# Optimization experiments

Hardware: AMD Instinct MI355X
Metric: run time of the kernel (lower is better)

## Reference

```python
import jax, jax.numpy as jnp
import numpy as np

N_NODES = 100000
N_EDGES = 1600000
IN_CH = 128
HID = 128
OUT_CH = 16
N_GRAPHS = 64


def setup_inputs() -> dict:
    key = jax.random.key(0)
    ks = jax.random.split(key, 8)
    x = jax.random.normal(ks[0], (N_NODES, IN_CH), dtype=jnp.float32)
    edge_index = jax.random.randint(ks[1], (2, N_EDGES), 0, N_NODES, dtype=jnp.int64)
    batch = jnp.sort(jax.random.randint(ks[2], (N_NODES,), 0, N_GRAPHS, dtype=jnp.int64))
    s1 = 1.0 / np.sqrt(IN_CH)
    s2 = 1.0 / np.sqrt(HID)
    W1 = jax.random.uniform(ks[3], (IN_CH, HID), jnp.float32, -s1, s1)
    b1 = jnp.zeros((HID,), jnp.float32)
    W2 = jax.random.uniform(ks[4], (HID, HID), jnp.float32, -s2, s2)
    b2 = jnp.zeros((HID,), jnp.float32)
    Wfc = jax.random.uniform(ks[5], (HID, OUT_CH), jnp.float32, -s2, s2)
    bfc = jax.random.uniform(ks[6], (OUT_CH,), jnp.float32, -s2, s2)
    return {"x": x, "W1": W1, "b1": b1, "W2": W2, "b2": b2,
            "Wfc": Wfc, "bfc": bfc, "edge_index": edge_index, "batch": batch}


def _gcn_conv(x, W, b, src, dst, deg_inv_sqrt, deg_inv):
    # GCNConv with self-loops: out = D^-1/2 (A+I) D^-1/2 (x W) + b
    h = x @ W                                   # [N, H]
    norm = deg_inv_sqrt[src] * deg_inv_sqrt[dst]  # [E]
    agg = jax.ops.segment_sum(h[src] * norm[:, None], dst, num_segments=N_NODES)
    # self-loop term: deg_inv_sqrt[i]^2 * h[i]
    return agg + h * deg_inv[:, None] + b


def reference(x, W1, b1, W2, b2, Wfc, bfc, edge_index, batch):
    src, dst = edge_index[0], edge_index[1]
    # degree including self-loop
    deg = jax.ops.segment_sum(jnp.ones((N_EDGES,), jnp.float32), dst, num_segments=N_NODES) + 1.0
    deg_inv_sqrt = jax.lax.rsqrt(deg)
    deg_inv = 1.0 / deg
    h = jax.nn.relu(_gcn_conv(x, W1, b1, src, dst, deg_inv_sqrt, deg_inv))
    h = jax.nn.relu(_gcn_conv(h, W2, b2, src, dst, deg_inv_sqrt, deg_inv))
    # global mean pool over graphs
    sums = jax.ops.segment_sum(h, batch, num_segments=N_GRAPHS)          # [G, H]
    counts = jax.ops.segment_sum(jnp.ones((N_NODES,), jnp.float32), batch, num_segments=N_GRAPHS)
    pooled = sums / jnp.maximum(counts, 1.0)[:, None]
    return pooled @ Wfc + bfc
```

## Files before the change

### kernel.cpp

```cpp
#include <hip/hip_runtime.h>
#include <math.h>

#define NN 100000
#define NE 1600000
#define CH 128
#define OUTC 16
#define NG 64

#define CBSH 9
#define NCB 196
#define CHK 8192
#define MAXB 12288
#define PS 8

typedef __attribute__((ext_vector_type(8))) short bf16x8;
typedef __attribute__((ext_vector_type(4))) float f32x4;

__device__ __forceinline__ unsigned short f2bf(float f) {
    union { float f; unsigned u; } v; v.f = f;
    unsigned r = v.u + 0x7FFF + ((v.u >> 16) & 1);
    return (unsigned short)(r >> 16);
}
__device__ __forceinline__ float bflo(unsigned u) {
    union { unsigned u; float f; } v; v.u = u << 16; return v.f;
}
__device__ __forceinline__ float bfhi(unsigned u) {
    union { unsigned u; float f; } v; v.u = u & 0xffff0000u; return v.f;
}

__global__ void k_prep(const float* __restrict__ W1, const float* __restrict__ W2,
                       unsigned short* __restrict__ wt1, unsigned short* __restrict__ wt2,
                       const int* __restrict__ batch, int* __restrict__ gptr,
                       int* __restrict__ bcnt) {
    int i = blockIdx.x * 256 + threadIdx.x;
    if (i < CH * CH) {
        int k = i >> 7, n = i & 127;
        wt1[n * CH + k] = f2bf(W1[i]);
    } else if (i < 2 * CH * CH) {
        int j = i - CH * CH;
        int k = j >> 7, n = j & 127;
        wt2[n * CH + k] = f2bf(W2[j]);
    }
    if (i < NCB) bcnt[i] = 0;
    if (i < NN) {
        int b = batch[i];
        int prev = (i == 0) ? -1 : batch[i - 1];
        for (int g = prev + 1; g <= b; g++) gptr[g] = i;
        if (i == NN - 1) {
            for (int g = b + 1; g <= NG; g++) gptr[g] = NN;
        }
    }
}

__global__ __launch_bounds__(1024) void k_hist(const int* __restrict__ dst, int* __restrict__ bcnt) {
    __shared__ int h[NCB];
    int t = threadIdx.x;
    if (t < NCB) h[t] = 0;
    __syncthreads();
    int base = blockIdx.x * CHK;
#pragma unroll
    for (int i = 0; i < 8; i++) {
        int e = base + i * 1024 + t;
        if (e < NE) atomicAdd(&h[dst[e] >> CBSH], 1);
    }
    __syncthreads();
    if (t < NCB && h[t]) atomicAdd(&bcnt[t], h[t]);
}

__global__ __launch_bounds__(1024) void k_bscan(const int* __restrict__ bcnt, int* __restrict__ ebase,
                        int* __restrict__ gfill, float* __restrict__ pooled) {
    __shared__ int s[256];
    int t = threadIdx.x;
    if (t < 256) s[t] = (t < NCB) ? bcnt[t] : 0;
    __syncthreads();
    for (int off = 1; off < 256; off <<= 1) {
        int v = 0;
        if (t < 256 && t >= off) v = s[t - off];
        __syncthreads();
        if (t < 256) s[t] += v;
        __syncthreads();
    }
    if (t == 0) ebase[0] = 0;
    if (t < NCB) { ebase[t + 1] = s[t]; gfill[t] = 0; }
    for (int i = t; i < NG * CH; i += 1024) pooled[i] = 0.f;
}

__global__ __launch_bounds__(1024) void k_passA(const int* __restrict__ src, const int* __restrict__ dst,
                        const int* __restrict__ ebase, int* __restrict__ gfill,
                        unsigned* __restrict__ ebuf) {
    __shared__ unsigned lbuf[CHK];
    __shared__ unsigned char lbyte[CHK];
    __shared__ int hcnt[NCB];
    __shared__ int hbase[256];
    __shared__ int goff[NCB];
    int t = threadIdx.x;
    if (t < NCB) hcnt[t] = 0;
    __syncthreads();
    int base = blockIdx.x * CHK;
    int cb[8], slot[8]; unsigned pk[8];
#pragma unroll
    for (int i = 0; i < 8; i++) {
        int e = base + i * 1024 + t;
        cb[i] = -1;
        if (e < NE) {
            int d = dst[e], s = src[e];
            cb[i] = d >> CBSH;
            pk[i] = ((unsigned)s << CBSH) | (unsigned)(d & 511);
            slot[i] = atomicAdd(&hcnt[cb[i]], 1);
        }
    }
    __syncthreads();
    if (t < 256) hbase[t] = (t < NCB) ? hcnt[t] : 0;
    __syncthreads();
    for (int off = 1; off < 256; off <<= 1) {
        int v = 0;
        if (t < 256 && t >= off) v = hbase[t - off];
        __syncthreads();
        if (t < 256) hbase[t] += v;
        __syncthreads();
    }
    if (t < NCB) {
        int c = hcnt[t];
        int g = c ? atomicAdd(&gfill[t], c) : 0;
        goff[t] = ebase[t] + g - (hbase[t] - c);
    }
    __syncthreads();
#pragma unroll
    for (int i = 0; i < 8; i++) {
        if (cb[i] >= 0) {
            int pos = hbase[cb[i]] - hcnt[cb[i]] + slot[i];
            lbuf[pos] = pk[i];
            lbyte[pos] = (unsigned char)cb[i];
        }
    }
    __syncthreads();
    int total = min(NE - base, CHK);
    for (int p = t; p < total; p += 1024) {
        unsigned v = lbuf[p];
        int b = lbyte[p];
        ebuf[goff[b] + p] = v;
    }
}

__global__ __launch_bounds__(1024) void k_passB(const unsigned* __restrict__ ebuf, const int* __restrict__ ebase,
                        int* __restrict__ degi, int* __restrict__ rowst,
                        float* __restrict__ dis, int* __restrict__ csr) {
    __shared__ int cnt[512];
    __shared__ int nbase[512];
    __shared__ int fill[512];
    __shared__ int stage[MAXB];
    int t = threadIdx.x;
    int cb = blockIdx.x;
    int nb0 = cb << CBSH;
    int ncnt = min(512, NN - nb0);
    int e0 = ebase[cb], e1 = ebase[cb + 1];
    if (t < 512) { cnt[t] = 0; fill[t] = 0; }
    __syncthreads();
    for (int e = e0 + t; e < e1; e += 1024)
        atomicAdd(&cnt[ebuf[e] & 511], 1);
    __syncthreads();
    if (t < 512) nbase[t] = cnt[t];
    __syncthreads();
    for (int off = 1; off < 512; off <<= 1) {
        int v = 0;
        if (t < 512 && t >= off) v = nbase[t - off];
        __syncthreads();
        if (t < 512) nbase[t] += v;
        __syncthreads();
    }
    for (int e = e0 + t; e < e1; e += 1024) {
        unsigned v = ebuf[e];
        int local = v & 511;
        int s = atomicAdd(&fill[local], 1);
        stage[nbase[local] - cnt[local] + s] = (int)(v >> CBSH);
    }
    __syncthreads();
    int total = e1 - e0;
    for (int p = t; p < total; p += 1024) csr[e0 + p] = stage[p];
    if (t < ncnt) {
        int c = cnt[t];
        degi[nb0 + t] = c;
        rowst[nb0 + t] = e0 + nbase[t] - c;
        dis[nb0 + t] = rsqrtf((float)c + 1.0f);
    }
}

template<bool F32IN>
__launch_bounds__(256, 2)
__global__ void k_gemm(const void* __restrict__ Av,
                       const unsigned short* __restrict__ WT,
                       const float* __restrict__ dis,
                       unsigned short* __restrict__ out) {
    int tid = threadIdx.x;
    int wave = tid >> 6, lane = tid & 63;
    int quad = lane >> 4, l16 = lane & 15;

    int rbase = blockIdx.x * 128 + wave * 32;

    bf16x8 af[2][4];
#pragma unroll
    for (int s = 0; s < 2; s++) {
        int row = rbase + s * 16 + l16;
        if (row >= NN) row = NN - 1;
        if (F32IN) {
            const float* arow = (const float*)Av + (size_t)row * CH + quad * 8;
#pragma unroll
            for (int ks = 0; ks < 4; ks++) {
                float4 lo = *(const float4*)(arow + ks * 32);
                float4 hi = *(const float4*)(arow + ks * 32 + 4);
                union { bf16x8 v; unsigned short u[8]; } tmp;
                tmp.u[0] = f2bf(lo.x); tmp.u[1] = f2bf(lo.y);
                tmp.u[2] = f2bf(lo.z); tmp.u[3] = f2bf(lo.w);
                tmp.u[4] = f2bf(hi.x); tmp.u[5] = f2bf(hi.y);
                tmp.u[6] = f2bf(hi.z); tmp.u[7] = f2bf(hi.w);
                af[s][ks] = tmp.v;
            }
        } else {
            const unsigned short* arow = (const unsigned short*)Av + (size_t)row * CH + quad * 8;
#pragma unroll
            for (int ks = 0; ks < 4; ks++) af[s][ks] = *(const bf16x8*)(arow + ks * 32);
        }
    }

    f32x4 acc[2][8];
#pragma unroll
    for (int s = 0; s < 2; s++)
#pragma unroll
        for (int t = 0; t < 8; t++) acc[s][t] = (f32x4){0.f, 0.f, 0.f, 0.f};

#pragma unroll
    for (int t = 0; t < 8; t++) {
        const unsigned short* wcol = WT + (size_t)(t * 16 + l16) * CH + quad * 8;
        bf16x8 b0 = *(const bf16x8*)(wcol);
        bf16x8 b1 = *(const bf16x8*)(wcol + 32);
        bf16x8 b2 = *(const bf16x8*)(wcol + 64);
        bf16x8 b3 = *(const bf16x8*)(wcol + 96);
#pragma unroll
        for (int s = 0; s < 2; s++) {
            acc[s][t] = __builtin_amdgcn_mfma_f32_16x16x32_bf16(af[s][0], b0, acc[s][t], 0, 0, 0);
            acc[s][t] = __builtin_amdgcn_mfma_f32_16x16x32_bf16(af[s][1], b1, acc[s][t], 0, 0, 0);
            acc[s][t] = __builtin_amdgcn_mfma_f32_16x16x32_bf16(af[s][2], b2, acc[s][t], 0, 0, 0);
            acc[s][t] = __builtin_amdgcn_mfma_f32_16x16x32_bf16(af[s][3], b3, acc[s][t], 0, 0, 0);
        }
    }

#pragma unroll
    for (int s = 0; s < 2; s++) {
#pragma unroll
        for (int r = 0; r < 4; r++) {
            int orow = rbase + s * 16 + quad * 4 + r;
            if (orow < NN) {
                float d = dis[orow];
#pragma unroll
                for (int t = 0; t < 8; t++) {
                    out[(size_t)orow * CH + t * 16 + l16] = f2bf(acc[s][t][r] * d);
                }
            }
        }
    }
}

__global__ __launch_bounds__(256) void k_agg(const unsigned short* __restrict__ ht, const int* __restrict__ rowst,
                      const int* __restrict__ degi, const int* __restrict__ csr,
                      const float* __restrict__ dis, const float* __restrict__ bias,
                      unsigned short* __restrict__ out) {
    int t = threadIdx.x;
    int grp = t >> 4;
    int q = t & 15;
    int n = blockIdx.x * 16 + grp;
    const uint4* base = (const uint4*)ht;

    uint4 sv = base[(size_t)n * 16 + q];
    float a[8];
    a[0] = bflo(sv.x); a[1] = bfhi(sv.x);
    a[2] = bflo(sv.y); a[3] = bfhi(sv.y);
    a[4] = bflo(sv.z); a[5] = bfhi(sv.z);
    a[6] = bflo(sv.w); a[7] = bfhi(sv.w);

    int start = rowst[n];
    int c = degi[n];
    int nb = c & ~7;
    int j = 0;
    for (; j < nb; j += 8) {
        int idx[8];
#pragma unroll
        for (int u = 0; u < 8; u++) idx[u] = csr[start + j + u];
        uint4 v[8];
#pragma unroll
        for (int u = 0; u < 8; u++) v[u] = base[(size_t)idx[u] * 16 + q];
#pragma unroll
        for (int u = 0; u < 8; u++) {
            a[0] += bflo(v[u].x); a[1] += bfhi(v[u].x);
            a[2] += bflo(v[u].y); a[3] += bfhi(v[u].y);
            a[4] += bflo(v[u].z); a[5] += bfhi(v[u].z);
            a[6] += bflo(v[u].w); a[7] += bfhi(v[u].w);
        }
    }
    if (j < c) {
        int idx[8];
#pragma unroll
        for (int u = 0; u < 8; u++) { int e = j + u; idx[u] = csr[start + (e < c ? e : c - 1)]; }
        uint4 v[8];
#pragma unroll
        for (int u = 0; u < 8; u++) v[u] = base[(size_t)idx[u] * 16 + q];
#pragma unroll
        for (int u = 0; u < 8; u++) {
            if (j + u < c) {
                a[0] += bflo(v[u].x); a[1] += bfhi(v[u].x);
                a[2] += bflo(v[u].y); a[3] += bfhi(v[u].y);
                a[4] += bflo(v[u].z); a[5] += bfhi(v[u].z);
                a[6] += bflo(v[u].w); a[7] += bfhi(v[u].w);
            }
        }
    }

    float d = dis[n];
    const float4* bp = (const float4*)bias;
    float4 b0 = bp[q * 2], b1 = bp[q * 2 + 1];
    uint4 o;
    {
        float ox = fmaxf(fmaf(d, a[0], b0.x), 0.f), oy = fmaxf(fmaf(d, a[1], b0.y), 0.f);
        o.x = ((unsigned)f2bf(oy) << 16) | (unsigned)f2bf(ox);
        ox = fmaxf(fmaf(d, a[2], b0.z), 0.f); oy = fmaxf(fmaf(d, a[3], b0.w), 0.f);
        o.y = ((unsigned)f2bf(oy) << 16) | (unsigned)f2bf(ox);
        ox = fmaxf(fmaf(d, a[4], b1.x), 0.f); oy = fmaxf(fmaf(d, a[5], b1.y), 0.f);
        o.z = ((unsigned)f2bf(oy) << 16) | (unsigned)f2bf(ox);
        ox = fmaxf(fmaf(d, a[6], b1.z), 0.f); oy = fmaxf(fmaf(d, a[7], b1.w), 0.f);
        o.w = ((unsigned)f2bf(oy) << 16) | (unsigned)f2bf(ox);
    }
    ((uint4*)out)[(size_t)n * 16 + q] = o;
}

__global__ __launch_bounds__(512) void k_pool2(const unsigned short* __restrict__ h,
                                               const int* __restrict__ gptr,
                                               float* __restrict__ pooled) {
    int g = blockIdx.x >> 3;
    int s = blockIdx.x & 7;
    int gs = gptr[g], ge = gptr[g + 1];
    int len = ge - gs;
    int i0 = gs + (int)(((long long)len * s) >> 3);
    int i1 = gs + (int)(((long long)len * (s + 1)) >> 3);
    int t = threadIdx.x;
    int pr = t & 63;
    int ro = t >> 6;
    const unsigned* base = (const unsigned*)h;
    float s0 = 0.f, s1 = 0.f;
    for (int n = i0 + ro; n < i1; n += 8) {
        unsigned v = base[(size_t)n * 64 + pr];
        s0 += bflo(v); s1 += bfhi(v);
    }
    __shared__ float red[2][8][64];
    red[0][ro][pr] = s0; red[1][ro][pr] = s1;
    __syncthreads();
    for (int off = 4; off >= 1; off >>= 1) {
        if (ro < off) {
            red[0][ro][pr] += red[0][ro + off][pr];
            red[1][ro][pr] += red[1][ro + off][pr];
        }
        __syncthreads();
    }
    if (ro == 0) {
        atomicAdd(&pooled[g * CH + pr * 2],     red[0][0][pr]);
        atomicAdd(&pooled[g * CH + pr * 2 + 1], red[1][0][pr]);
    }
}

__global__ void k_final(const float* __restrict__ pooled, const int* __restrict__ gptr,
                        const float* __restrict__ Wfc, const float* __restrict__ bfc,
                        float* __restrict__ out) {
    int idx = blockIdx.x * 256 + threadIdx.x;
    if (idx >= NG * OUTC) return;
    int g = idx >> 4, o = idx & 15;
    float c = (float)(gptr[g + 1] - gptr[g]);
    float inv = 1.0f / fmaxf(c, 1.0f);
    float s = 0.f;
    for (int k = 0; k < CH; k++) s += pooled[g * CH + k] * Wfc[k * OUTC + o];
    out[idx] = fmaf(s, inv, bfc[o]);
}

extern "C" void kernel_launch(void* const* d_in, const int* in_sizes, int n_in,
                              void* d_out, int out_size, void* d_ws, size_t ws_size,
                              hipStream_t stream) {
    (void)in_sizes; (void)n_in; (void)out_size; (void)ws_size;
    const float* x   = (const float*)d_in[0];
    const float* W1  = (const float*)d_in[1];
    const float* b1  = (const float*)d_in[2];
    const float* W2  = (const float*)d_in[3];
    const float* b2  = (const float*)d_in[4];
    const float* Wfc = (const float*)d_in[5];
    const float* bfc = (const float*)d_in[6];
    const int* ei    = (const int*)d_in[7];
    const int* batch = (const int*)d_in[8];
    const int* esrc = ei;
    const int* edst = ei + NE;
    float* out = (float*)d_out;

    char* w = (char*)d_ws;
    unsigned short* bufA = (unsigned short*)w; w += (size_t)NN * CH * 2;
    unsigned short* bufB = (unsigned short*)w; w += (size_t)NN * CH * 2;
    unsigned short* wt1  = (unsigned short*)w; w += (size_t)CH * CH * 2;
    unsigned short* wt2  = (unsigned short*)w; w += (size_t)CH * CH * 2;
    unsigned* ebuf = (unsigned*)w; w += (size_t)NE * 4;
    int* csr    = (int*)w;    w += (size_t)NE * 4;
    int* degi   = (int*)w;    w += (size_t)NN * 4;
    int* rowst  = (int*)w;    w += (size_t)NN * 4;
    float* dis  = (float*)w;  w += (size_t)NN * 4;
    int* bcnt   = (int*)w;    w += NCB * 4;
    int* ebase  = (int*)w;    w += (NCB + 1) * 4;
    int* gfill  = (int*)w;    w += NCB * 4;
    int* gptr   = (int*)w;    w += (NG + 1) * 4;
    float* pooled = (float*)w; w += (size_t)NG * CH * 4;

    const int histBlocks = (NE + CHK - 1) / CHK;
    const int gemmBlocks = (NN + 127) / 128;
    const int aggBlocks  = NN / 16;

    k_prep<<<(NN + 255) / 256, 256, 0, stream>>>(W1, W2, wt1, wt2, batch, gptr, bcnt);
    k_hist<<<histBlocks, 1024, 0, stream>>>(edst, bcnt);
    k_bscan<<<1, 1024, 0, stream>>>(bcnt, ebase, gfill, pooled);
    k_passA<<<histBlocks, 1024, 0, stream>>>(esrc, edst, ebase, gfill, ebuf);
    k_passB<<<NCB, 1024, 0, stream>>>(ebuf, ebase, degi, rowst, dis, csr);

    k_gemm<true><<<gemmBlocks, 256, 0, stream>>>(x, wt1, dis, bufA);
    k_agg<<<aggBlocks, 256, 0, stream>>>(bufA, rowst, degi, csr, dis, b1, bufB);
    k_gemm<false><<<gemmBlocks, 256, 0, stream>>>(bufB, wt2, dis, bufA);
    k_agg<<<aggBlocks, 256, 0, stream>>>(bufA, rowst, degi, csr, dis, b2, bufB);

    k_pool2<<<NG * PS, 512, 0, stream>>>(bufB, gptr, pooled);
    k_final<<<(NG * OUTC + 255) / 256, 256, 0, stream>>>(pooled, gptr, Wfc, bfc, out);
}
```

Baseline: 319.2 us.

## Fuse layer-1 GEMM, edge histogram and prep into one heterogeneous launch

Merges the first-layer GEMM (with W1 transposed and converted into shared memory per block), the destination-bucket histogram (now written as per-block partials), and the prep work into a single kernel whose blocks pick a role by block index. The layer-1 GEMM no longer depends on the CSR build or on dis, so it runs alongside the edge preprocessing. A new aggregation variant k_agg_w applies the source-side dis weights per edge, since the GEMM output is now unscaled. The cost is that every GEMM block redoes the W1 transpose into LDS, and the single-block bscan now has to sum 196 partial histograms.

```diff
diff --git a/kernel.cpp b/kernel.cpp
--- a/kernel.cpp
+++ b/kernel.cpp
@@ -12,6 +12,11 @@
 #define CHK 8192
 #define MAXB 12288
 #define PS 8
+#define LDA 136
+
+#define GEMMB 782
+#define HISTB 196
+#define PREPB 391
 
 typedef __attribute__((ext_vector_type(8))) short bf16x8;
 typedef __attribute__((ext_vector_type(4))) float f32x4;
@@ -28,182 +33,37 @@
     union { unsigned u; float f; } v; v.u = u & 0xffff0000u; return v.f;
 }
 
-__global__ void k_prep(const float* __restrict__ W1, const float* __restrict__ W2,
-                       unsigned short* __restrict__ wt1, unsigned short* __restrict__ wt2,
-                       const int* __restrict__ batch, int* __restrict__ gptr,
-                       int* __restrict__ bcnt) {
-    int i = blockIdx.x * 256 + threadIdx.x;
-    if (i < CH * CH) {
-        int k = i >> 7, n = i & 127;
-        wt1[n * CH + k] = f2bf(W1[i]);
-    } else if (i < 2 * CH * CH) {
-        int j = i - CH * CH;
-        int k = j >> 7, n = j & 127;
-        wt2[n * CH + k] = f2bf(W2[j]);
-    }
-    if (i < NCB) bcnt[i] = 0;
-    if (i < NN) {
-        int b = batch[i];
-        int prev = (i == 0) ? -1 : batch[i - 1];
-        for (int g = prev + 1; g <= b; g++) gptr[g] = i;
-        if (i == NN - 1) {
-            for (int g = b + 1; g <= NG; g++) gptr[g] = NN;
-        }
-    }
-}
-
-__global__ __launch_bounds__(1024) void k_hist(const int* __restrict__ dst, int* __restrict__ bcnt) {
-    __shared__ int h[NCB];
-    int t = threadIdx.x;
-    if (t < NCB) h[t] = 0;
-    __syncthreads();
-    int base = blockIdx.x * CHK;
-#pragma unroll
-    for (int i = 0; i < 8; i++) {
-        int e = base + i * 1024 + t;
-        if (e < NE) atomicAdd(&h[dst[e] >> CBSH], 1);
-    }
-    __syncthreads();
-    if (t < NCB && h[t]) atomicAdd(&bcnt[t], h[t]);
-}
-
-__global__ __launch_bounds__(1024) void k_bscan(const int* __restrict__ bcnt, int* __restrict__ ebase,
-                        int* __restrict__ gfill, float* __restrict__ pooled) {
-    __shared__ int s[256];
-    int t = threadIdx.x;
-    if (t < 256) s[t] = (t < NCB) ? bcnt[t] : 0;
-    __syncthreads();
-    for (int off = 1; off < 256; off <<= 1) {
-        int v = 0;
-        if (t < 256 && t >= off) v = s[t - off];
-        __syncthreads();
-        if (t < 256) s[t] += v;
-        __syncthreads();
-    }
-    if (t == 0) ebase[0] = 0;
-    if (t < NCB) { ebase[t + 1] = s[t]; gfill[t] = 0; }
-    for (int i = t; i < NG * CH; i += 1024) pooled[i] = 0.f;
-}
-
-__global__ __launch_bounds__(1024) void k_passA(const int* __restrict__ src, const int* __restrict__ dst,
-                        const int* __restrict__ ebase, int* __restrict__ gfill,
-                        unsigned* __restrict__ ebuf) {
-    __shared__ unsigned lbuf[CHK];
-    __shared__ unsigned char lbyte[CHK];
-    __shared__ int hcnt[NCB];
-    __shared__ int hbase[256];
-    __shared__ int goff[NCB];
-    int t = threadIdx.x;
-    if (t < NCB) hcnt[t] = 0;
-    __syncthreads();
-    int base = blockIdx.x * CHK;
-    int cb[8], slot[8]; unsigned pk[8];
-#pragma unroll
-    for (int i = 0; i < 8; i++) {
-        int e = base + i * 1024 + t;
-        cb[i] = -1;
-        if (e < NE) {
-            int d = dst[e], s = src[e];
-            cb[i] = d >> CBSH;
-            pk[i] = ((unsigned)s << CBSH) | (unsigned)(d & 511);
-            slot[i] = atomicAdd(&hcnt[cb[i]], 1);
-        }
-    }
-    __syncthreads();
-    if (t < 256) hbase[t] = (t < NCB) ? hcnt[t] : 0;
-    __syncthreads();
-    for (int off = 1; off < 256; off <<= 1) {
-        int v = 0;
-        if (t < 256 && t >= off) v = hbase[t - off];
-        __syncthreads();
-        if (t < 256) hbase[t] += v;
-        __syncthreads();
-    }
-    if (t < NCB) {
-        int c = hcnt[t];
-        int g = c ? atomicAdd(&gfill[t], c) : 0;
-        goff[t] = ebase[t] + g - (hbase[t] - c);
-    }
-    __syncthreads();
-#pragma unroll
-    for (int i = 0; i < 8; i++) {
-        if (cb[i] >= 0) {
-            int pos = hbase[cb[i]] - hcnt[cb[i]] + slot[i];
-            lbuf[pos] = pk[i];
-            lbyte[pos] = (unsigned char)cb[i];
-        }
-    }
-    __syncthreads();
-    int total = min(NE - base, CHK);
-    for (int p = t; p < total; p += 1024) {
-        unsigned v = lbuf[p];
-        int b = lbyte[p];
-        ebuf[goff[b] + p] = v;
-    }
-}
-
-__global__ __launch_bounds__(1024) void k_passB(const unsigned* __restrict__ ebuf, const int* __restrict__ ebase,
-                        int* __restrict__ degi, int* __restrict__ rowst,
-                        float* __restrict__ dis, int* __restrict__ csr) {
-    __shared__ int cnt[512];
-    __shared__ int nbase[512];
-    __shared__ int fill[512];
-    __shared__ int stage[MAXB];
-    int t = threadIdx.x;
-    int cb = blockIdx.x;
-    int nb0 = cb << CBSH;
-    int ncnt = min(512, NN - nb0);
-    int e0 = ebase[cb], e1 = ebase[cb + 1];
-    if (t < 512) { cnt[t] = 0; fill[t] = 0; }
-    __syncthreads();
-    for (int e = e0 + t; e < e1; e += 1024)
-        atomicAdd(&cnt[ebuf[e] & 511], 1);
-    __syncthreads();
-    if (t < 512) nbase[t] = cnt[t];
-    __syncthreads();
-    for (int off = 1; off < 512; off <<= 1) {
-        int v = 0;
-        if (t < 512 && t >= off) v = nbase[t - off];
-        __syncthreads();
-        if (t < 512) nbase[t] += v;
-        __syncthreads();
-    }
-    for (int e = e0 + t; e < e1; e += 1024) {
-        unsigned v = ebuf[e];
-        int local = v & 511;
-        int s = atomicAdd(&fill[local], 1);
-        stage[nbase[local] - cnt[local] + s] = (int)(v >> CBSH);
-    }
-    __syncthreads();
-    int total = e1 - e0;
-    for (int p = t; p < total; p += 1024) csr[e0 + p] = stage[p];
-    if (t < ncnt) {
-        int c = cnt[t];
-        degi[nb0 + t] = c;
-        rowst[nb0 + t] = e0 + nbase[t] - c;
-        dis[nb0 + t] = rsqrtf((float)c + 1.0f);
-    }
-}
-
-template<bool F32IN>
 __launch_bounds__(256, 2)
-__global__ void k_gemm(const void* __restrict__ Av,
-                       const unsigned short* __restrict__ WT,
-                       const float* __restrict__ dis,
-                       unsigned short* __restrict__ out) {
-    int tid = threadIdx.x;
-    int wave = tid >> 6, lane = tid & 63;
-    int quad = lane >> 4, l16 = lane & 15;
-
-    int rbase = blockIdx.x * 128 + wave * 32;
-
-    bf16x8 af[2][4];
-#pragma unroll
-    for (int s = 0; s < 2; s++) {
-        int row = rbase + s * 16 + l16;
-        if (row >= NN) row = NN - 1;
-        if (F32IN) {
-            const float* arow = (const float*)Av + (size_t)row * CH + quad * 8;
+__global__ void k_fused0(const float* __restrict__ x, const float* __restrict__ W1,
+                         const float* __restrict__ W2,
+                         unsigned short* __restrict__ wt2,
+                         const int* __restrict__ batch, int* __restrict__ gptr,
+                         int* __restrict__ gfill, float* __restrict__ pooled,
+                         const int* __restrict__ edst, int* __restrict__ hpart,
+                         unsigned short* __restrict__ bufA) {
+    __shared__ unsigned short wlds[128 * LDA];
+    int b = blockIdx.x;
+    int t = threadIdx.x;
+
+    if (b < GEMMB) {
+#pragma unroll
+        for (int it = 0; it < 64; it++) {
+            int i = it * 256 + t;
+            int k = i >> 7, n = i & 127;
+            wlds[n * LDA + k] = f2bf(W1[i]);
+        }
+        __syncthreads();
+
+        int wave = t >> 6, lane = t & 63;
+        int quad = lane >> 4, l16 = lane & 15;
+        int rbase = b * 128 + wave * 32;
+
+        bf16x8 af[2][4];
+#pragma unroll
+        for (int s = 0; s < 2; s++) {
+            int row = rbase + s * 16 + l16;
+            if (row >= NN) row = NN - 1;
+            const float* arow = x + (size_t)row * CH + quad * 8;
 #pragma unroll
             for (int ks = 0; ks < 4; ks++) {
                 float4 lo = *(const float4*)(arow + ks * 32);
@@ -215,11 +75,288 @@
                 tmp.u[6] = f2bf(hi.z); tmp.u[7] = f2bf(hi.w);
                 af[s][ks] = tmp.v;
             }
-        } else {
-            const unsigned short* arow = (const unsigned short*)Av + (size_t)row * CH + quad * 8;
-#pragma unroll
-            for (int ks = 0; ks < 4; ks++) af[s][ks] = *(const bf16x8*)(arow + ks * 32);
-        }
+        }
+
+        f32x4 acc[2][8];
+#pragma unroll
+        for (int s = 0; s < 2; s++)
+#pragma unroll
+            for (int tt = 0; tt < 8; tt++) acc[s][tt] = (f32x4){0.f, 0.f, 0.f, 0.f};
+
+#pragma unroll
+        for (int tt = 0; tt < 8; tt++) {
+            const unsigned short* wcol = &wlds[(tt * 16 + l16) * LDA + quad * 8];
+            bf16x8 b0 = *(const bf16x8*)(wcol);
+            bf16x8 b1 = *(const bf16x8*)(wcol + 32);
+            bf16x8 b2 = *(const bf16x8*)(wcol + 64);
+            bf16x8 b3 = *(const bf16x8*)(wcol + 96);
+#pragma unroll
+            for (int s = 0; s < 2; s++) {
+                acc[s][tt] = __builtin_amdgcn_mfma_f32_16x16x32_bf16(af[s][0], b0, acc[s][tt], 0, 0, 0);
+                acc[s][tt] = __builtin_amdgcn_mfma_f32_16x16x32_bf16(af[s][1], b1, acc[s][tt], 0, 0, 0);
+                acc[s][tt] = __builtin_amdgcn_mfma_f32_16x16x32_bf16(af[s][2], b2, acc[s][tt], 0, 0, 0);
+                acc[s][tt] = __builtin_amdgcn_mfma_f32_16x16x32_bf16(af[s][3], b3, acc[s][tt], 0, 0, 0);
+            }
+        }
+
+#pragma unroll
+        for (int s = 0; s < 2; s++) {
+#pragma unroll
+            for (int r = 0; r < 4; r++) {
+                int orow = rbase + s * 16 + quad * 4 + r;
+                if (orow < NN) {
+#pragma unroll
+                    for (int tt = 0; tt < 8; tt++)
+                        bufA[(size_t)orow * CH + tt * 16 + l16] = f2bf(acc[s][tt][r]);
+                }
+            }
+        }
+    } else if (b < GEMMB + HISTB) {
+        int* h = (int*)wlds;
+        if (t < NCB) h[t] = 0;
+        __syncthreads();
+        int hb = b - GEMMB;
+        int base = hb * CHK;
+#pragma unroll
+        for (int i = 0; i < 32; i++) {
+            int e = base + i * 256 + t;
+            if (e < NE) atomicAdd(&h[edst[e] >> CBSH], 1);
+        }
+        __syncthreads();
+        if (t < NCB) hpart[hb * NCB + t] = h[t];
+    } else {
+        int i = (b - GEMMB - HISTB) * 256 + t;
+        if (i < CH * CH) {
+            int k = i >> 7, n = i & 127;
+            wt2[n * CH + k] = f2bf(W2[i]);
+        }
+        if (i < NCB) gfill[i] = 0;
+        if (i < NG * CH) pooled[i] = 0.f;
+        if (i < NN) {
+            int bb = batch[i];
+            int prev = (i == 0) ? -1 : batch[i - 1];
+            for (int g = prev + 1; g <= bb; g++) gptr[g] = i;
+            if (i == NN - 1) {
+                for (int g = bb + 1; g <= NG; g++) gptr[g] = NN;
+            }
+        }
+    }
+}
+
+__global__ __launch_bounds__(256) void k_bscan(const int* __restrict__ hpart,
+                                               int* __restrict__ ebase) {
+    __shared__ int s[256];
+    int t = threadIdx.x;
+    int sum = 0;
+    if (t < NCB)
+        for (int b = 0; b < HISTB; b++) sum += hpart[b * NCB + t];
+    s[t] = (t < NCB) ? sum : 0;
+    __syncthreads();
+    for (int off = 1; off < 256; off <<= 1) {
+        int v = 0;
+        if (t >= off) v = s[t - off];
+        __syncthreads();
+        s[t] += v;
+        __syncthreads();
+    }
+    if (t == 0) ebase[0] = 0;
+    if (t < NCB) ebase[t + 1] = s[t];
+}
+
+__global__ __launch_bounds__(1024) void k_passA(const int* __restrict__ src, const int* __restrict__ dst,
+                        const int* __restrict__ ebase, int* __restrict__ gfill,
+                        unsigned* __restrict__ ebuf) {
+    __shared__ unsigned lbuf[CHK];
+    __shared__ unsigned char lbyte[CHK];
+    __shared__ int hcnt[NCB];
+    __shared__ int hbase[256];
+    __shared__ int goff[NCB];
+    int t = threadIdx.x;
+    if (t < NCB) hcnt[t] = 0;
+    __syncthreads();
+    int base = blockIdx.x * CHK;
+    int cb[8], slot[8]; unsigned pk[8];
+#pragma unroll
+    for (int i = 0; i < 8; i++) {
+        int e = base + i * 1024 + t;
+        cb[i] = -1;
+        if (e < NE) {
+            int d = dst[e], s = src[e];
+            cb[i] = d >> CBSH;
+            pk[i] = ((unsigned)s << CBSH) | (unsigned)(d & 511);
+            slot[i] = atomicAdd(&hcnt[cb[i]], 1);
+        }
+    }
+    __syncthreads();
+    if (t < 256) hbase[t] = (t < NCB) ? hcnt[t] : 0;
+    __syncthreads();
+    for (int off = 1; off < 256; off <<= 1) {
+        int v = 0;
+        if (t < 256 && t >= off) v = hbase[t - off];
+        __syncthreads();
+        if (t < 256) hbase[t] += v;
+        __syncthreads();
+    }
+    if (t < NCB) {
+        int c = hcnt[t];
+        int g = c ? atomicAdd(&gfill[t], c) : 0;
+        goff[t] = ebase[t] + g - (hbase[t] - c);
+    }
+    __syncthreads();
+#pragma unroll
+    for (int i = 0; i < 8; i++) {
+        if (cb[i] >= 0) {
+            int pos = hbase[cb[i]] - hcnt[cb[i]] + slot[i];
+            lbuf[pos] = pk[i];
+            lbyte[pos] = (unsigned char)cb[i];
+        }
+    }
+    __syncthreads();
+    int total = min(NE - base, CHK);
+    for (int p = t; p < total; p += 1024) {
+        unsigned v = lbuf[p];
+        int b = lbyte[p];
+        ebuf[goff[b] + p] = v;
+    }
+}
+
+__global__ __launch_bounds__(1024) void k_passB(const unsigned* __restrict__ ebuf, const int* __restrict__ ebase,
+                        int* __restrict__ degi, int* __restrict__ rowst,
+                        float* __restrict__ dis, int* __restrict__ csr) {
+    __shared__ int cnt[512];
+    __shared__ int nbase[512];
+    __shared__ int fill[512];
+    __shared__ int stage[MAXB];
+    int t = threadIdx.x;
+    int cb = blockIdx.x;
+    int nb0 = cb << CBSH;
+    int ncnt = min(512, NN - nb0);
+    int e0 = ebase[cb], e1 = ebase[cb + 1];
+    if (t < 512) { cnt[t] = 0; fill[t] = 0; }
+    __syncthreads();
+    for (int e = e0 + t; e < e1; e += 1024)
+        atomicAdd(&cnt[ebuf[e] & 511], 1);
+    __syncthreads();
+    if (t < 512) nbase[t] = cnt[t];
+    __syncthreads();
+    for (int off = 1; off < 512; off <<= 1) {
+        int v = 0;
+        if (t < 512 && t >= off) v = nbase[t - off];
+        __syncthreads();
+        if (t < 512) nbase[t] += v;
+        __syncthreads();
+    }
+    for (int e = e0 + t; e < e1; e += 1024) {
+        unsigned v = ebuf[e];
+        int local = v & 511;
+        int s = atomicAdd(&fill[local], 1);
+        stage[nbase[local] - cnt[local] + s] = (int)(v >> CBSH);
+    }
+    __syncthreads();
+    int total = e1 - e0;
+    for (int p = t; p < total; p += 1024) csr[e0 + p] = stage[p];
+    if (t < ncnt) {
+        int c = cnt[t];
+        degi[nb0 + t] = c;
+        rowst[nb0 + t] = e0 + nbase[t] - c;
+        dis[nb0 + t] = rsqrtf((float)c + 1.0f);
+    }
+}
+
+__global__ __launch_bounds__(256) void k_agg_w(const unsigned short* __restrict__ ht, const int* __restrict__ rowst,
+                      const int* __restrict__ degi, const int* __restrict__ csr,
+                      const float* __restrict__ dis, const float* __restrict__ bias,
+                      unsigned short* __restrict__ out) {
+    int t = threadIdx.x;
+    int grp = t >> 4;
+    int q = t & 15;
+    int n = blockIdx.x * 16 + grp;
+    const uint4* base = (const uint4*)ht;
+
+    float d = dis[n];
+    uint4 sv = base[(size_t)n * 16 + q];
+    float a[8];
+    a[0] = d * bflo(sv.x); a[1] = d * bfhi(sv.x);
+    a[2] = d * bflo(sv.y); a[3] = d * bfhi(sv.y);
+    a[4] = d * bflo(sv.z); a[5] = d * bfhi(sv.z);
+    a[6] = d * bflo(sv.w); a[7] = d * bfhi(sv.w);
+
+    int start = rowst[n];
+    int c = degi[n];
+    int nb = c & ~7;
+    int j = 0;
+    for (; j < nb; j += 8) {
+        int idx[8];
+#pragma unroll
+        for (int u = 0; u < 8; u++) idx[u] = csr[start + j + u];
+        uint4 v[8]; float w[8];
+#pragma unroll
+        for (int u = 0; u < 8; u++) v[u] = base[(size_t)idx[u] * 16 + q];
+#pragma unroll
+        for (int u = 0; u < 8; u++) w[u] = dis[idx[u]];
+#pragma unroll
+        for (int u = 0; u < 8; u++) {
+            a[0] = fmaf(w[u], bflo(v[u].x), a[0]); a[1] = fmaf(w[u], bfhi(v[u].x), a[1]);
+            a[2] = fmaf(w[u], bflo(v[u].y), a[2]); a[3] = fmaf(w[u], bfhi(v[u].y), a[3]);
+            a[4] = fmaf(w[u], bflo(v[u].z), a[4]); a[5] = fmaf(w[u], bfhi(v[u].z), a[5]);
+            a[6] = fmaf(w[u], bflo(v[u].w), a[6]); a[7] = fmaf(w[u], bfhi(v[u].w), a[7]);
+        }
+    }
+    if (j < c) {
+        int idx[8];
+#pragma unroll
+        for (int u = 0; u < 8; u++) { int e = j + u; idx[u] = csr[start + (e < c ? e : c - 1)]; }
+        uint4 v[8]; float w[8];
+#pragma unroll
+        for (int u = 0; u < 8; u++) v[u] = base[(size_t)idx[u] * 16 + q];
+#pragma unroll
+        for (int u = 0; u < 8; u++) w[u] = dis[idx[u]];
+#pragma unroll
+        for (int u = 0; u < 8; u++) {
+            if (j + u < c) {
+                a[0] = fmaf(w[u], bflo(v[u].x), a[0]); a[1] = fmaf(w[u], bfhi(v[u].x), a[1]);
+                a[2] = fmaf(w[u], bflo(v[u].y), a[2]); a[3] = fmaf(w[u], bfhi(v[u].y), a[3]);
+                a[4] = fmaf(w[u], bflo(v[u].z), a[4]); a[5] = fmaf(w[u], bfhi(v[u].z), a[5]);
+                a[6] = fmaf(w[u], bflo(v[u].w), a[6]); a[7] = fmaf(w[u], bfhi(v[u].w), a[7]);
+            }
+        }
+    }
+
+    const float4* bp = (const float4*)bias;
+    float4 b0 = bp[q * 2], b1 = bp[q * 2 + 1];
+    uint4 o;
+    {
+        float ox = fmaxf(fmaf(d, a[0], b0.x), 0.f), oy = fmaxf(fmaf(d, a[1], b0.y), 0.f);
+        o.x = ((unsigned)f2bf(oy) << 16) | (unsigned)f2bf(ox);
+        ox = fmaxf(fmaf(d, a[2], b0.z), 0.f); oy = fmaxf(fmaf(d, a[3], b0.w), 0.f);
+        o.y = ((unsigned)f2bf(oy) << 16) | (unsigned)f2bf(ox);
+        ox = fmaxf(fmaf(d, a[4], b1.x), 0.f); oy = fmaxf(fmaf(d, a[5], b1.y), 0.f);
+        o.z = ((unsigned)f2bf(oy) << 16) | (unsigned)f2bf(ox);
+        ox = fmaxf(fmaf(d, a[6], b1.z), 0.f); oy = fmaxf(fmaf(d, a[7], b1.w), 0.f);
+        o.w = ((unsigned)f2bf(oy) << 16) | (unsigned)f2bf(ox);
+    }
+    ((uint4*)out)[(size_t)n * 16 + q] = o;
+}
+
+__launch_bounds__(256, 2)
+__global__ void k_gemm2(const unsigned short* __restrict__ Av,
+                        const unsigned short* __restrict__ WT,
+                        const float* __restrict__ dis,
+                        unsigned short* __restrict__ out) {
+    int tid = threadIdx.x;
+    int wave = tid >> 6, lane = tid & 63;
+    int quad = lane >> 4, l16 = lane & 15;
+
+    int rbase = blockIdx.x * 128 + wave * 32;
+
+    bf16x8 af[2][4];
+#pragma unroll
+    for (int s = 0; s < 2; s++) {
+        int row = rbase + s * 16 + l16;
+        if (row >= NN) row = NN - 1;
+        const unsigned short* arow = Av + (size_t)row * CH + quad * 8;
+#pragma unroll
+        for (int ks = 0; ks < 4; ks++) af[s][ks] = *(const bf16x8*)(arow + ks * 32);
     }
 
     f32x4 acc[2][8];
@@ -398,32 +535,30 @@
     char* w = (char*)d_ws;
     unsigned short* bufA = (unsigned short*)w; w += (size_t)NN * CH * 2;
     unsigned short* bufB = (unsigned short*)w; w += (size_t)NN * CH * 2;
-    unsigned short* wt1  = (unsigned short*)w; w += (size_t)CH * CH * 2;
     unsigned short* wt2  = (unsigned short*)w; w += (size_t)CH * CH * 2;
     unsigned* ebuf = (unsigned*)w; w += (size_t)NE * 4;
     int* csr    = (int*)w;    w += (size_t)NE * 4;
     int* degi   = (int*)w;    w += (size_t)NN * 4;
     int* rowst  = (int*)w;    w += (size_t)NN * 4;
     float* dis  = (float*)w;  w += (size_t)NN * 4;
-    int* bcnt   = (int*)w;    w += NCB * 4;
+    int* hpart  = (int*)w;    w += (size_t)HISTB * NCB * 4;
     int* ebase  = (int*)w;    w += (NCB + 1) * 4;
     int* gfill  = (int*)w;    w += NCB * 4;
     int* gptr   = (int*)w;    w += (NG + 1) * 4;
     float* pooled = (float*)w; w += (size_t)NG * CH * 4;
 
-    const int histBlocks = (NE + CHK - 1) / CHK;
+    const int fusedBlocks = GEMMB + HISTB + PREPB;
     const int gemmBlocks = (NN + 127) / 128;
     const int aggBlocks  = NN / 16;
 
-    k_prep<<<(NN + 255) / 256, 256, 0, stream>>>(W1, W2, wt1, wt2, batch, gptr, bcnt);
-    k_hist<<<histBlocks, 1024, 0, stream>>>(edst, bcnt);
-    k_bscan<<<1, 1024, 0, stream>>>(bcnt, ebase, gfill, pooled);
-    k_passA<<<histBlocks, 1024, 0, stream>>>(esrc, edst, ebase, gfill, ebuf);
+    k_fused0<<<fusedBlocks, 256, 0, stream>>>(x, W1, W2, wt2, batch, gptr, gfill,
+                                              pooled, edst, hpart, bufA);
+    k_bscan<<<1, 256, 0, stream>>>(hpart, ebase);
+    k_passA<<<HISTB, 1024, 0, stream>>>(esrc, edst, ebase, gfill, ebuf);
     k_passB<<<NCB, 1024, 0, stream>>>(ebuf, ebase, degi, rowst, dis, csr);
 
-    k_gemm<true><<<gemmBlocks, 256, 0, stream>>>(x, wt1, dis, bufA);
-    k_agg<<<aggBlocks, 256, 0, stream>>>(bufA, rowst, degi, csr, dis, b1, bufB);
-    k_gemm<false><<<gemmBlocks, 256, 0, stream>>>(bufB, wt2, dis, bufA);
+    k_agg_w<<<aggBlocks, 256, 0, stream>>>(bufA, rowst, degi, csr, dis, b1, bufB);
+    k_gemm2<<<gemmBlocks, 256, 0, stream>>>(bufB, wt2, dis, bufA);
     k_agg<<<aggBlocks, 256, 0, stream>>>(bufA, rowst, degi, csr, dis, b2, bufB);
 
     k_pool2<<<NG * PS, 512, 0, stream>>>(bufB, gptr, pooled);
```

New measurement: 313.7 us. No clear change (-1.7%).
